# Optimization experiments

Hardware: AMD Instinct MI355X
Metric: run time of the kernel (lower is better)

The kernel has to match this reference:

```python
import jax, jax.numpy as jnp
import numpy as np

NHEAD, DK, DV = 8, 32, 32
GRAPH = [[1,2,3,6,7],[1,2,4],[1,3,5],[2,4],[3,5],[1,6,8,12],[1,7,9,13],[6,8,10],[7,9,13],[8,10],[9,11],[9,12,14],[11,13,15],[12,14,16],[13,15,17],[14,16],[15,17]]
_idx = np.zeros((17,5), np.int32); _val = np.zeros((17,5), bool)
for _i, _nb in enumerate(GRAPH):
    for _j, _n in enumerate(_nb):
        _idx[_i,_j] = _n-1; _val[_i,_j] = True
NBR_IDX = jnp.asarray(_idx)            # (17,5) neighbor table (pad idx 0)
NBR_VALID = jnp.asarray(_val)          # (17,5) valid-neighbor mask
ATT_MASK = jnp.asarray(np.concatenate([_val, np.ones((17,2), bool)], 1))  # (17,7): 5 local + 2 global keys
INV_SQRT_DK = float(1.0/np.sqrt(DK))

def _ln_c(x, g, b, eps=1e-6):
    # LayerNorm over channel axis of (B,C,L)
    m = x.mean(1, keepdims=True)
    v = x.var(1, keepdims=True)
    return (x - m) * jax.lax.rsqrt(v + eps) * g[None,:,None] + b[None,:,None]

def _bn3(x, g, b, eps=1e-5):
    # BatchNorm1d (training batch stats) per channel over (B,L); x:(B,C,L)
    m = x.mean((0,2), keepdims=True)
    v = x.var((0,2), keepdims=True)
    return (x - m) * jax.lax.rsqrt(v + eps) * g[None,:,None] + b[None,:,None]

def _pos_ffn(x, w1, b1, w2, b2, g, b):
    # x:(B,C,L); Linear over C, relu, Linear back, residual, BatchNorm1d
    h = jax.nn.relu(jnp.einsum('bcl,hc->bhl', x, w1) + b1[None,:,None])
    y = jnp.einsum('bhl,ch->bcl', h, w2) + b2[None,:,None] + x
    return _bn3(y, g, b)

def _unfold(t):
    # t:(B,C,17) -> (B,C,5,17): per-node 5-wide neighbor window, zero padded
    g = t[:,:,NBR_IDX]                              # (B,C,17,5)
    g = jnp.where(NBR_VALID[None,None], g, 0.0)
    return jnp.transpose(g, (0,1,3,2))

def _sju(xn, ax, wq,bq,wk,bk,wv,bv, bng,bnb, f1w,f1b,f2w,f2b,fg,fb):
    B, C, L = xn.shape
    q = (jnp.einsum('oc,bcl->bol', wq, xn) + bq[None,:,None]).reshape(B,NHEAD,DK,L)
    kx = jnp.einsum('oc,bcl->bol', wk, xn) + bk[None,:,None]
    vx = jnp.einsum('oc,bcl->bol', wv, xn) + bv[None,:,None]
    k = _unfold(kx).reshape(B,NHEAD,DK,5,L)
    v = _unfold(vx).reshape(B,NHEAD,DV,5,L)
    ak = (jnp.einsum('oc,bcal->boal', wk, ax) + bk[None,:,None,None]).reshape(B,NHEAD,DK,2,L)
    av = (jnp.einsum('oc,bcal->boal', wv, ax) + bv[None,:,None,None]).reshape(B,NHEAD,DV,2,L)
    k = jnp.concatenate([k, ak], 3)                 # (B,H,dk,7,L)
    v = jnp.concatenate([v, av], 3)
    pre = jnp.einsum('bhdl,bhdwl->bhwl', q, k) * INV_SQRT_DK
    pre = jnp.where(ATT_MASK.T[None,None], pre, -jnp.inf)
    a = jax.nn.softmax(pre, axis=2)
    att = jnp.einsum('bhwl,bhdwl->bhdl', a, v).reshape(B,C,L)
    ret = _bn3(xn + att, bng, bnb)
    return _pos_ffn(ret, f1w,f1b,f2w,f2b,fg,fb)

def _sru(x, y, wq,bq,wk,bk,wv,bv, bng,bnb, f1w,f1b,f2w,f2b,fg,fb):
    # x:(B,C) relay, y:(B,C,Ly) keys/values
    B, C = x.shape
    q = (x @ wq.T + bq).reshape(B,NHEAD,DK)
    k = (jnp.einsum('oc,bcl->bol', wk, y) + bk[None,:,None]).reshape(B,NHEAD,DK,-1)
    v = (jnp.einsum('oc,bcl->bol', wv, y) + bv[None,:,None]).reshape(B,NHEAD,DV,-1)
    a = jax.nn.softmax(jnp.einsum('bhd,bhdl->bhl', q, k) * INV_SQRT_DK, axis=2)
    att = jnp.einsum('bhl,bhdl->bhd', a, v).reshape(B,C)
    ret = _bn3((x + att)[:,:,None], bng, bnb)
    return _pos_ffn(ret, f1w,f1b,f2w,f2b,fg,fb)[:,:,0]

def _forward(data, ln_g, ln_b, jq_w, jq_b, jk_w, jk_b, jv_w, jv_b, jbn_g, jbn_b, jf1_w, jf1_b, jf2_w, jf2_b, jfbn_g, jfbn_b, rq_w, rq_b, rk_w, rk_b, rv_w, rv_b, rbn_g, rbn_b, rf1_w, rf1_b, rf2_w, rf2_b, rfbn_g, rfbn_b):
    B, C, V, T = data.shape
    embs = jnp.transpose(data, (0,3,1,2)).reshape(B*T, C, V)   # fold time into batch
    nodes = embs
    relay = embs.mean(2)                                       # (BT,C)
    # ax: per node the 2 extra keys = its own original embedding + relay (fixed across layers)
    ax = jnp.stack([embs, jnp.broadcast_to(relay[:,:,None], embs.shape)], axis=2)  # (BT,C,2,V)
    for i in range(ln_g.shape[0]):
        xn = _ln_c(nodes, ln_g[i], ln_b[i])
        nodes = jax.nn.leaky_relu(_sju(xn, ax, jq_w[i],jq_b[i],jk_w[i],jk_b[i],jv_w[i],jv_b[i],jbn_g[i],jbn_b[i],jf1_w[i],jf1_b[i],jf2_w[i],jf2_b[i],jfbn_g[i],jfbn_b[i]), 0.01)
        y = jnp.concatenate([relay[:,:,None], nodes], axis=2)   # (BT,C,18)
        relay = jax.nn.leaky_relu(_sru(relay, y, rq_w[i],rq_b[i],rk_w[i],rk_b[i],rv_w[i],rv_b[i],rbn_g[i],rbn_b[i],rf1_w[i],rf1_b[i],rf2_w[i],rf2_b[i],rfbn_g[i],rfbn_b[i]), 0.01)
    return jnp.transpose(nodes.reshape(B,T,C,V), (0,2,3,1))

def setup_inputs():
    key = jax.random.key(0)
    Lyr, C, DIN, B, T, V = 2, 256, 1024, 4, 256, 17
    ks = jax.random.split(key, 40)
    ctr = [0]
    def nxt():
        k = ks[ctr[0]]; ctr[0] += 1; return k
    def w(shape, s=0.05):
        return jax.random.normal(nxt(), shape, jnp.float32) * s
    ones = lambda: jnp.ones((Lyr, C), jnp.float32)
    zeros = lambda: jnp.zeros((Lyr, C), jnp.float32)
    inp = {'data': jax.random.normal(nxt(), (B,C,V,T), jnp.float32),
           'ln_g': ones(), 'ln_b': zeros()}
    for p in ('j', 'r'):
        inp[p+'q_w'] = w((Lyr,C,C)); inp[p+'q_b'] = w((Lyr,C))
        inp[p+'k_w'] = w((Lyr,C,C)); inp[p+'k_b'] = w((Lyr,C))
        inp[p+'v_w'] = w((Lyr,C,C)); inp[p+'v_b'] = w((Lyr,C))
        inp[p+'bn_g'] = ones(); inp[p+'bn_b'] = zeros()
        inp[p+'f1_w'] = w((Lyr,DIN,C)); inp[p+'f1_b'] = w((Lyr,DIN))
        inp[p+'f2_w'] = w((Lyr,C,DIN)); inp[p+'f2_b'] = w((Lyr,C))
        inp[p+'fbn_g'] = ones(); inp[p+'fbn_b'] = zeros()
    return inp

def reference(data, ln_g, ln_b, jq_w, jq_b, jk_w, jk_b, jv_w, jv_b, jbn_g, jbn_b, jf1_w, jf1_b, jf2_w, jf2_b, jfbn_g, jfbn_b, rq_w, rq_b, rk_w, rk_b, rv_w, rv_b, rbn_g, rbn_b, rf1_w, rf1_b, rf2_w, rf2_b, rfbn_g, rfbn_b):
    return _forward(data, ln_g, ln_b, jq_w, jq_b, jk_w, jk_b, jv_w, jv_b, jbn_g, jbn_b, jf1_w, jf1_b, jf2_w, jf2_b, jfbn_g, jfbn_b, rq_w, rq_b, rk_w, rk_b, rv_w, rv_b, rbn_g, rbn_b, rf1_w, rf1_b, rf2_w, rf2_b, rfbn_g, rfbn_b)
```

## Files before the change

kernel.cpp:

```cpp
#include <hip/hip_runtime.h>
#include <hip/hip_bf16.h>


using bf16 = __hip_bfloat16;
typedef __attribute__((ext_vector_type(8))) short bf16x8v;
typedef __attribute__((ext_vector_type(4))) float f32x4;

namespace {
constexpr int kBT = 1024;
constexpr int kC = 256;
constexpr int kV = 17;
constexpr int kT = 256;
constexpr int kDIN = 1024;
constexpr int kRows = kBT * kV;
constexpr int kRowsE = kRows + kBT;
constexpr float kInvSqrtDk = 0.17677669529663687f;
constexpr size_t SZ_BIG = (size_t)kRows * kC;
}

__constant__ int c_nbi[17][5] = {
    {0, 1, 2, 5, 6},   {0, 1, 3, 0, 0},   {0, 2, 4, 0, 0},  {1, 3, 0, 0, 0},
    {2, 4, 0, 0, 0},   {0, 5, 7, 11, 0},  {0, 6, 8, 12, 0}, {5, 7, 9, 0, 0},
    {6, 8, 12, 0, 0},  {7, 9, 0, 0, 0},   {8, 10, 0, 0, 0}, {8, 11, 13, 0, 0},
    {10, 12, 14, 0, 0},{11, 13, 15, 0, 0},{12, 14, 16, 0, 0},
    {13, 15, 0, 0, 0}, {14, 16, 0, 0, 0}};
__constant__ int c_ncnt[17] = {5, 3, 3, 2, 2, 4, 4, 3, 3, 2, 2, 3, 3, 3, 3, 2, 2};

__device__ inline float bf2f(unsigned short s) {
  unsigned int u = ((unsigned int)s) << 16;
  float f;
  __builtin_memcpy(&f, &u, 4);
  return f;
}
__device__ inline unsigned short f2bf(float f) {
  unsigned int u;
  __builtin_memcpy(&u, &f, 4);
  unsigned int r = (u + 0x7fffu + ((u >> 16) & 1u)) >> 16;
  return (unsigned short)r;
}
__device__ inline float4 ldbf4(const bf16* p) {
  ushort4 u = *(const ushort4*)p;
  return make_float4(bf2f(u.x), bf2f(u.y), bf2f(u.z), bf2f(u.w));
}
__device__ inline void stbf4(bf16* p, float4 v) {
  ushort4 u = make_ushort4(f2bf(v.x), f2bf(v.y), f2bf(v.z), f2bf(v.w));
  *(ushort4*)p = u;
}
__device__ inline float dot4(float4 a, float4 b) {
  return a.x * b.x + a.y * b.y + a.z * b.z + a.w * b.w;
}

__device__ inline void async16(const bf16* g, bf16* l) {
  __builtin_amdgcn_global_load_lds(
      (const __attribute__((address_space(1))) void*)g,
      (__attribute__((address_space(3))) void*)l, 16, 0, 0);
}

template <int KT>
__device__ __forceinline__ void gemm128_body(
    char* smem_raw, const bf16* __restrict__ A, const bf16* __restrict__ W,
    const float* __restrict__ bias, bf16* __restrict__ outB, int N, int flags,
    int row0, int col0) {
  bf16* As = (bf16*)smem_raw;
  bf16* Bs = (bf16*)(smem_raw + 16384);
  const int tid = threadIdx.x;
  const int wave = tid >> 6;
  const int lane = tid & 63;

  const int sub = lane >> 2;
  const int kq = (lane & 3) * 8;
  const int rg0 = (2 * wave + 0) * 16;
  const int rg1 = (2 * wave + 1) * 16;
  const bf16* ag0 = A + (size_t)(row0 + rg0 + sub) * KT + kq;
  const bf16* ag1 = A + (size_t)(row0 + rg1 + sub) * KT + kq;
  const bf16* bg0 = W + (size_t)(col0 + rg0 + sub) * KT + kq;
  const bf16* bg1 = W + (size_t)(col0 + rg1 + sub) * KT + kq;

  const int wm = wave >> 1, wn = wave & 1;
  const int fr = lane & 15;
  const int fk = (lane >> 4) * 8;

  f32x4 acc[4][4];
#pragma unroll
  for (int i = 0; i < 4; ++i)
#pragma unroll
    for (int j = 0; j < 4; ++j) acc[i][j] = (f32x4){0.f, 0.f, 0.f, 0.f};

#define STAGE32(buf, koff)                              \
  do {                                                  \
    async16(ag0 + (koff), As + (buf) * 4096 + rg0 * 32); \
    async16(ag1 + (koff), As + (buf) * 4096 + rg1 * 32); \
    async16(bg0 + (koff), Bs + (buf) * 4096 + rg0 * 32); \
    async16(bg1 + (koff), Bs + (buf) * 4096 + rg1 * 32); \
  } while (0)

  STAGE32(0, 0);
  __syncthreads();

  for (int k0 = 0; k0 < KT; k0 += 32) {
    const int cur = (k0 >> 5) & 1;
    if (k0 + 32 < KT) STAGE32(cur ^ 1, k0 + 32);
    bf16x8v af[4], bfv[4];
#pragma unroll
    for (int i = 0; i < 4; ++i)
      af[i] = *(const bf16x8v*)&As[cur * 4096 +
                                   (wm * 64 + i * 16 + fr) * 32 + fk];
#pragma unroll
    for (int j = 0; j < 4; ++j)
      bfv[j] = *(const bf16x8v*)&Bs[cur * 4096 +
                                    (wn * 64 + j * 16 + fr) * 32 + fk];
#pragma unroll
    for (int i = 0; i < 4; ++i)
#pragma unroll
      for (int j = 0; j < 4; ++j)
        acc[i][j] = __builtin_amdgcn_mfma_f32_16x16x32_bf16(af[i], bfv[j],
                                                            acc[i][j], 0, 0,
                                                            0);
    __syncthreads();
  }
#undef STAGE32

  unsigned short* cs = (unsigned short*)smem_raw;
#pragma unroll
  for (int j = 0; j < 4; ++j) {
    int lc = wn * 64 + j * 16 + fr;
    float bv = bias ? bias[col0 + lc] : 0.f;
#pragma unroll
    for (int i = 0; i < 4; ++i) {
      int lr = wm * 64 + i * 16 + (lane >> 4) * 4;
#pragma unroll
      for (int r = 0; r < 4; ++r) {
        float v = acc[i][j][r] + bv;
        if (flags & 1) v = fmaxf(v, 0.f);
        cs[(lr + r) * 128 + lc] = f2bf(v);
      }
    }
  }
  __syncthreads();
#pragma unroll
  for (int p = 0; p < 8; ++p) {
    int lr = p * 16 + (tid >> 4);
    int lc = (tid & 15) * 8;
    *(bf16x8v*)&outB[(size_t)(row0 + lr) * N + col0 + lc] =
        *(const bf16x8v*)&cs[lr * 128 + lc];
  }
}

template <int KT>
__global__ __launch_bounds__(256, 4) void k_mfma_gemm(
    const bf16* __restrict__ A, const bf16* __restrict__ W,
    const float* __restrict__ bias, bf16* __restrict__ outB, int N,
    int flags) {
  __shared__ __align__(16) char smem_raw[32768];
  gemm128_body<KT>(smem_raw, A, W, bias, outB, N, flags, blockIdx.x * 128,
                   blockIdx.y * 128);
}

__global__ __launch_bounds__(256, 4) void k_mfma_gemm_dual(
    const bf16* __restrict__ A0, const bf16* __restrict__ W0,
    const float* __restrict__ b0, bf16* __restrict__ o0, int N0, int gx0,
    int nb0, const bf16* __restrict__ A1, const bf16* __restrict__ W1,
    const float* __restrict__ b1, bf16* __restrict__ o1, int N1, int gx1) {
  __shared__ __align__(16) char smem_raw[32768];
  const int bid = blockIdx.x;
  if (bid < nb0) {
    int bx = bid % gx0, by = bid / gx0;
    gemm128_body<256>(smem_raw, A0, W0, b0, o0, N0, 4, bx * 128, by * 128);
  } else {
    int local = bid - nb0;
    int bx = local % gx1, by = local / gx1;
    gemm128_body<256>(smem_raw, A1, W1, b1, o1, N1, 4, bx * 128, by * 128);
  }
}

__global__ __launch_bounds__(256, 4) void k_mfma_gemm64(
    const bf16* __restrict__ A, const bf16* __restrict__ W,
    const float* __restrict__ bias, const float* __restrict__ res,
    float* __restrict__ outF, const float* __restrict__ bnScI,
    const float* __restrict__ bnShI, float* __restrict__ partOut, int nbPart,
    int N) {
  constexpr int KT = 1024;
  __shared__ __align__(16) bf16 As[2][4096];
  __shared__ __align__(16) bf16 Bs[2][4096];
  __shared__ float sred[4 * 64];
  __shared__ float qred[4 * 64];
  const int tid = threadIdx.x;
  const int wave = tid >> 6;
  const int lane = tid & 63;
  const int row0 = blockIdx.x * 64;
  const int col0 = blockIdx.y * 64;

  const int srow = wave * 16 + (lane >> 2);
  const int skq = (lane & 3) * 8;
  const bf16* ag = A + (size_t)(row0 + srow) * KT + skq;
  const bf16* bg = W + (size_t)(col0 + srow) * KT + skq;

  const int wm = wave >> 1, wn = wave & 1;
  const int fr = lane & 15;
  const int fk = (lane >> 4) * 8;

  f32x4 acc[2][2];
#pragma unroll
  for (int i = 0; i < 2; ++i)
#pragma unroll
    for (int j = 0; j < 2; ++j) acc[i][j] = (f32x4){0.f, 0.f, 0.f, 0.f};

#define STAGE64x64(buf, koff)                                      \
  do {                                                             \
    _Pragma("unroll") for (int kc = 0; kc < 2; ++kc) {             \
      async16(ag + (koff) + kc * 32,                               \
              &As[(buf)][kc * 2048 + wave * 512]);                 \
      async16(bg + (koff) + kc * 32,                               \
              &Bs[(buf)][kc * 2048 + wave * 512]);                 \
    }                                                              \
  } while (0)

  STAGE64x64(0, 0);
  __syncthreads();

  for (int k0 = 0; k0 < KT; k0 += 64) {
    const int cur = (k0 >> 6) & 1;
    if (k0 + 64 < KT) STAGE64x64(cur ^ 1, k0 + 64);
#pragma unroll
    for (int kc = 0; kc < 2; ++kc) {
      bf16x8v af[2], bfv[2];
#pragma unroll
      for (int i = 0; i < 2; ++i)
        af[i] = *(const bf16x8v*)&As[cur][kc * 2048 +
                                          (wm * 32 + i * 16 + fr) * 32 + fk];
#pragma unroll
      for (int j = 0; j < 2; ++j)
        bfv[j] = *(const bf16x8v*)&Bs[cur][kc * 2048 +
                                           (wn * 32 + j * 16 + fr) * 32 + fk];
#pragma unroll
      for (int i = 0; i < 2; ++i)
#pragma unroll
        for (int j = 0; j < 2; ++j)
          acc[i][j] = __builtin_amdgcn_mfma_f32_16x16x32_bf16(af[i], bfv[j],
                                                              acc[i][j], 0, 0,
                                                              0);
    }
    __syncthreads();
  }
#undef STAGE64x64

  const int crow = row0 + wm * 32;
  const int ccol = col0 + wn * 32;
  float colS[2] = {0.f, 0.f};
  float colQ[2] = {0.f, 0.f};
#pragma unroll
  for (int j = 0; j < 2; ++j) {
    int col = ccol + j * 16 + fr;
    float bv = bias[col];
    float rsc = bnScI[col], rsh = bnShI[col];
#pragma unroll
    for (int i = 0; i < 2; ++i) {
      int rowb = crow + i * 16 + (lane >> 4) * 4;
#pragma unroll
      for (int r = 0; r < 4; ++r) {
        size_t row = (size_t)(rowb + r);
        float v = acc[i][j][r] + bv + res[row * N + col] * rsc + rsh;
        outF[row * N + col] = v;
        colS[j] += v;
        colQ[j] += v * v;
      }
    }
  }
#pragma unroll
  for (int j = 0; j < 2; ++j) {
    colS[j] += __shfl_xor(colS[j], 16);
    colS[j] += __shfl_xor(colS[j], 32);
    colQ[j] += __shfl_xor(colQ[j], 16);
    colQ[j] += __shfl_xor(colQ[j], 32);
  }
  if (lane < 16) {
#pragma unroll
    for (int j = 0; j < 2; ++j) {
      sred[wave * 64 + j * 16 + fr] = colS[j];
      qred[wave * 64 + j * 16 + fr] = colQ[j];
    }
  }
  __syncthreads();
  if (tid < 64) {
    int c = tid;
    int wsel = c >> 5, off = c & 31;
    float s = sred[wsel * 64 + off] + sred[(wsel + 2) * 64 + off];
    float q = qred[wsel * 64 + off] + qred[(wsel + 2) * 64 + off];
    int col = col0 + c;
    partOut[(size_t)blockIdx.x * kC + col] = s;
    partOut[(size_t)(nbPart + blockIdx.x) * kC + col] = q;
  }
}

__global__ __launch_bounds__(256) void k_xform_in(const float* __restrict__ data,
                                                  float* __restrict__ nodes,
                                                  bf16* __restrict__ embs_bf) {
  __shared__ float tile[32][33];
  int ct = blockIdx.x * 32, tt = blockIdx.y * 32;
  int bv = blockIdx.z;
  int b = bv / kV, v = bv - b * kV;
  int tx = threadIdx.x & 31, ty = threadIdx.x >> 5;
  for (int i = ty; i < 32; i += 8)
    tile[i][tx] = data[(((size_t)b * kC + ct + i) * kV + v) * kT + tt + tx];
  __syncthreads();
  for (int i = ty; i < 32; i += 8) {
    size_t s = (size_t)b * kT + tt + i;
    size_t idx = (s * kV + v) * kC + ct + tx;
    float val = tile[tx][i];
    nodes[idx] = val;
    embs_bf[idx] = __float2bfloat16(val);
  }
}

__global__ __launch_bounds__(256) void k_xform_out(const float* __restrict__ Z,
                                                   const float* __restrict__ scale,
                                                   const float* __restrict__ shift,
                                                   float* __restrict__ out) {
  __shared__ float tile[32][33];
  int ct = blockIdx.x * 32, tt = blockIdx.y * 32;
  int bv = blockIdx.z;
  int b = bv / kV, v = bv - b * kV;
  int tx = threadIdx.x & 31, ty = threadIdx.x >> 5;
  float sc = scale[ct + tx], sh = shift[ct + tx];
  for (int i = ty; i < 32; i += 8) {
    size_t s = (size_t)b * kT + tt + i;
    float val = Z[(s * kV + v) * kC + ct + tx] * sc + sh;
    val = (val > 0.f) ? val : 0.01f * val;
    tile[i][tx] = val;
  }
  __syncthreads();
  for (int i = ty; i < 32; i += 8)
    out[(((size_t)b * kC + ct + i) * kV + v) * kT + tt + tx] = tile[tx][i];
}

__global__ __launch_bounds__(256) void k_ln_relay(
    const float* __restrict__ nodes, const float* __restrict__ g,
    const float* __restrict__ b, float* __restrict__ O,
    bf16* __restrict__ Ob, bf16* __restrict__ relay0_bf) {
  int t = threadIdx.x;
  int bid = blockIdx.x;
  if (bid < kRows / 4) {
    int row = bid * 4 + (t >> 6);
    int c4 = (t & 63) * 4;
    size_t i = (size_t)row * kC + c4;
    float4 x = *(const float4*)(nodes + i);
    float s = x.x + x.y + x.z + x.w;
    float q = dot4(x, x);
#pragma unroll
    for (int o = 32; o >= 1; o >>= 1) {
      s += __shfl_xor(s, o);
      q += __shfl_xor(q, o);
    }
    float m = s * (1.f / 256.f);
    float var = q * (1.f / 256.f) - m * m;
    float rs = rsqrtf(var + 1e-6f);
    float4 g4 = *(const float4*)(g + c4);
    float4 b4 = *(const float4*)(b + c4);
    float4 o4 = make_float4((x.x - m) * rs * g4.x + b4.x,
                            (x.y - m) * rs * g4.y + b4.y,
                            (x.z - m) * rs * g4.z + b4.z,
                            (x.w - m) * rs * g4.w + b4.w);
    *(float4*)(O + i) = o4;
    stbf4(Ob + i, o4);
  } else {
    int s = (bid - kRows / 4) * 4 + (t >> 6);
    int c4 = (t & 63) * 4;
    float4 acc = make_float4(0.f, 0.f, 0.f, 0.f);
#pragma unroll
    for (int v = 0; v < kV; ++v) {
      float4 x = *(const float4*)(nodes + ((size_t)s * kV + v) * kC + c4);
      acc.x += x.x; acc.y += x.y; acc.z += x.z; acc.w += x.w;
    }
    float4 r =
        make_float4(acc.x / 17.f, acc.y / 17.f, acc.z / 17.f, acc.w / 17.f);
    stbf4(relay0_bf + (size_t)s * kC + c4, r);
  }
}

__global__ __launch_bounds__(256) void k_attn_sat(const bf16* __restrict__ qkv,
                                                  const bf16* __restrict__ akav,
                                                  float* __restrict__ z,
                                                  float* __restrict__ part,
                                                  int nb) {
  __shared__ float sS[4][256];
  __shared__ float qS[4][256];
  int t = threadIdx.x;
  int w = t >> 6;
  int lane = t & 63;
  int c4 = lane * 4;
  float sAcc[4] = {0.f, 0.f, 0.f, 0.f};
  float qAcc[4] = {0.f, 0.f, 0.f, 0.f};
  for (int r = 0; r < 4; ++r) {
    int rl = blockIdx.x * 16 + w * 4 + r;
    int s = rl / kV, l = rl - s * kV;
    float4 q = ldbf4(qkv + (size_t)rl * 768 + c4);
    int cnt = c_ncnt[l];
    float sc[7];
    int nrow[5];
#pragma unroll
    for (int wd = 0; wd < 5; ++wd) {
      nrow[wd] = s * kV + c_nbi[l][wd];
      float4 k = ldbf4(qkv + (size_t)nrow[wd] * 768 + 256 + c4);
      float p = dot4(q, k);
      p += __shfl_xor(p, 1, 8);
      p += __shfl_xor(p, 2, 8);
      p += __shfl_xor(p, 4, 8);
      sc[wd] = (wd < cnt) ? p * kInvSqrtDk : -1e30f;
    }
    {
      float4 k = ldbf4(akav + (size_t)rl * 1024 + c4);
      float p = dot4(q, k);
      p += __shfl_xor(p, 1, 8);
      p += __shfl_xor(p, 2, 8);
      p += __shfl_xor(p, 4, 8);
      sc[5] = p * kInvSqrtDk;
    }
    {
      float4 k = ldbf4(akav + (size_t)(kRows + s) * 1024 + c4);
      float p = dot4(q, k);
      p += __shfl_xor(p, 1, 8);
      p += __shfl_xor(p, 2, 8);
      p += __shfl_xor(p, 4, 8);
      sc[6] = p * kInvSqrtDk;
    }
    float mx = sc[0];
#pragma unroll
    for (int wd = 1; wd < 7; ++wd) mx = fmaxf(mx, sc[wd]);
    float den = 0.f;
#pragma unroll
    for (int wd = 0; wd < 7; ++wd) {
      sc[wd] = __expf(sc[wd] - mx);
      den += sc[wd];
    }
    float inv = 1.f / den;
    float4 acc = make_float4(0.f, 0.f, 0.f, 0.f);
#pragma unroll
    for (int wd = 0; wd < 5; ++wd) {
      float4 v = ldbf4(qkv + (size_t)nrow[wd] * 768 + 512 + c4);
      acc.x += sc[wd] * v.x; acc.y += sc[wd] * v.y;
      acc.z += sc[wd] * v.z; acc.w += sc[wd] * v.w;
    }
    {
      float4 v = ldbf4(akav + (size_t)rl * 1024 + 256 + c4);
      acc.x += sc[5] * v.x; acc.y += sc[5] * v.y;
      acc.z += sc[5] * v.z; acc.w += sc[5] * v.w;
    }
    {
      float4 v = ldbf4(akav + (size_t)(kRows + s) * 1024 + 256 + c4);
      acc.x += sc[6] * v.x; acc.y += sc[6] * v.y;
      acc.z += sc[6] * v.z; acc.w += sc[6] * v.w;
    }
    size_t zi = (size_t)rl * kC + c4;
    float4 xv = *(const float4*)(z + zi);
    float4 o = make_float4(xv.x + acc.x * inv, xv.y + acc.y * inv,
                           xv.z + acc.z * inv, xv.w + acc.w * inv);
    *(float4*)(z + zi) = o;
    sAcc[0] += o.x; sAcc[1] += o.y; sAcc[2] += o.z; sAcc[3] += o.w;
    qAcc[0] += o.x * o.x; qAcc[1] += o.y * o.y;
    qAcc[2] += o.z * o.z; qAcc[3] += o.w * o.w;
  }
  sS[w][c4 + 0] = sAcc[0]; sS[w][c4 + 1] = sAcc[1];
  sS[w][c4 + 2] = sAcc[2]; sS[w][c4 + 3] = sAcc[3];
  qS[w][c4 + 0] = qAcc[0]; qS[w][c4 + 1] = qAcc[1];
  qS[w][c4 + 2] = qAcc[2]; qS[w][c4 + 3] = qAcc[3];
  __syncthreads();
  float ps = sS[0][t] + sS[1][t] + sS[2][t] + sS[3][t];
  float pq = qS[0][t] + qS[1][t] + qS[2][t] + qS[3][t];
  part[(size_t)blockIdx.x * kC + t] = ps;
  part[(size_t)(nb + blockIdx.x) * kC + t] = pq;
}

__global__ __launch_bounds__(256) void k_bn_finalize(const float* __restrict__ part,
                                                     int nb, float inv_n,
                                                     const float* __restrict__ g,
                                                     const float* __restrict__ b,
                                                     float* __restrict__ scale,
                                                     float* __restrict__ shift) {
  int c = blockIdx.x;
  int t = threadIdx.x;
  float s = 0.f, q = 0.f;
  for (int i = t; i < nb; i += 256) {
    s += part[(size_t)i * kC + c];
    q += part[(size_t)(nb + i) * kC + c];
  }
#pragma unroll
  for (int o = 32; o >= 1; o >>= 1) {
    s += __shfl_xor(s, o);
    q += __shfl_xor(q, o);
  }
  __shared__ float ws[4], wq[4];
  int wid = t >> 6;
  if ((t & 63) == 0) { ws[wid] = s; wq[wid] = q; }
  __syncthreads();
  if (t == 0) {
    float S = ws[0] + ws[1] + ws[2] + ws[3];
    float Q = wq[0] + wq[1] + wq[2] + wq[3];
    float m = S * inv_n;
    float var = Q * inv_n - m * m;
    float sc = g[c] * rsqrtf(var + 1e-5f);
    scale[c] = sc;
    shift[c] = b[c] - m * sc;
  }
}

__global__ __launch_bounds__(256) void k_bn_apply(const float* __restrict__ Z,
                                                  const float* __restrict__ scale,
                                                  const float* __restrict__ shift,
                                                  float* __restrict__ outF,
                                                  bf16* __restrict__ outB,
                                                  int leaky) {
  int t = threadIdx.x;
  int row = blockIdx.x * 4 + (t >> 6);
  int c4 = (t & 63) * 4;
  size_t i = (size_t)row * kC + c4;
  float4 z = *(const float4*)(Z + i);
  float4 sc = *(const float4*)(scale + c4);
  float4 sh = *(const float4*)(shift + c4);
  float4 v = make_float4(z.x * sc.x + sh.x, z.y * sc.y + sh.y,
                         z.z * sc.z + sh.z, z.w * sc.w + sh.w);
  if (leaky) {
    v.x = (v.x > 0.f) ? v.x : 0.01f * v.x;
    v.y = (v.y > 0.f) ? v.y : 0.01f * v.y;
    v.z = (v.z > 0.f) ? v.z : 0.01f * v.z;
    v.w = (v.w > 0.f) ? v.w : 0.01f * v.w;
  }
  if (outF) *(float4*)(outF + i) = v;
  if (outB) stbf4(outB + i, v);
}

__global__ __launch_bounds__(256) void k_bn_ln(
    const float* __restrict__ Z, const float* __restrict__ scale,
    const float* __restrict__ shift, const float* __restrict__ g,
    const float* __restrict__ b, float* __restrict__ xnOut,
    bf16* __restrict__ actOut) {
  int t = threadIdx.x;
  int row = blockIdx.x * 4 + (t >> 6);
  int c4 = (t & 63) * 4;
  size_t i = (size_t)row * kC + c4;
  float4 z = *(const float4*)(Z + i);
  float4 sc = *(const float4*)(scale + c4);
  float4 sh = *(const float4*)(shift + c4);
  float4 v = make_float4(z.x * sc.x + sh.x, z.y * sc.y + sh.y,
                         z.z * sc.z + sh.z, z.w * sc.w + sh.w);
  v.x = (v.x > 0.f) ? v.x : 0.01f * v.x;
  v.y = (v.y > 0.f) ? v.y : 0.01f * v.y;
  v.z = (v.z > 0.f) ? v.z : 0.01f * v.z;
  v.w = (v.w > 0.f) ? v.w : 0.01f * v.w;
  float s = v.x + v.y + v.z + v.w;
  float q = dot4(v, v);
#pragma unroll
  for (int o = 32; o >= 1; o >>= 1) {
    s += __shfl_xor(s, o);
    q += __shfl_xor(q, o);
  }
  float m = s * (1.f / 256.f);
  float var = q * (1.f / 256.f) - m * m;
  float rs = rsqrtf(var + 1e-6f);
  float4 g4 = *(const float4*)(g + c4);
  float4 b4 = *(const float4*)(b + c4);
  float4 o4 = make_float4((v.x - m) * rs * g4.x + b4.x,
                          (v.y - m) * rs * g4.y + b4.y,
                          (v.z - m) * rs * g4.z + b4.z,
                          (v.w - m) * rs * g4.w + b4.w);
  *(float4*)(xnOut + i) = o4;
  stbf4(actOut + i, o4);
}

struct CvtTab {
  const float* src[12];
  bf16* dst[12];
  int n[12];
  const float* bsrc[10];
  float* bdst[10];
};
__global__ __launch_bounds__(256) void k_cvt_multi(CvtTab t) {
  int c = blockIdx.y;
  if (c == 12) {
    if (blockIdx.x < 10) t.bdst[blockIdx.x][threadIdx.x] = t.bsrc[blockIdx.x][threadIdx.x];
    return;
  }
  int i = (blockIdx.x * 256 + threadIdx.x) * 4;
  if (i >= t.n[c]) return;
  float4 v = *(const float4*)(t.src[c] + i);
  stbf4(t.dst[c] + i, v);
}

extern "C" void kernel_launch(void* const* d_in, const int* in_sizes, int n_in,
                              void* d_out, int out_size, void* d_ws, size_t ws_size,
                              hipStream_t stream) {
  const float* data = (const float*)d_in[0];
  const float* ln_g = (const float*)d_in[1];
  const float* ln_b = (const float*)d_in[2];
  const float* jq_w = (const float*)d_in[3];
  const float* jq_b = (const float*)d_in[4];
  const float* jk_w = (const float*)d_in[5];
  const float* jk_b = (const float*)d_in[6];
  const float* jv_w = (const float*)d_in[7];
  const float* jv_b = (const float*)d_in[8];
  const float* jbn_g = (const float*)d_in[9];
  const float* jbn_b = (const float*)d_in[10];
  const float* jf1_w = (const float*)d_in[11];
  const float* jf1_b = (const float*)d_in[12];
  const float* jf2_w = (const float*)d_in[13];
  const float* jf2_b = (const float*)d_in[14];
  const float* jfbn_g = (const float*)d_in[15];
  const float* jfbn_b = (const float*)d_in[16];
  float* out = (float*)d_out;

  float* f = (float*)d_ws;
  float* nodes = f;    f += SZ_BIG;
  float* xn = f;       f += SZ_BIG;
  float* part = f;     f += 2 * (kRows / 4) * kC;
  float* scale = f;    f += kC;
  float* shift = f;    f += kC;
  float* cb_jqkv = f;  f += 2 * 768;
  float* cb_kv4 = f;   f += 1024;

  bf16* bfa = (bf16*)f;
  bf16* act_bf = bfa;   bfa += SZ_BIG;
  bf16* embsX_bf = bfa; bfa += (size_t)kRowsE * kC;
  bf16* P = bfa;        bfa += (size_t)kRows * kDIN;
  bf16* akavBuf = bfa;  bfa += (size_t)kRowsE * 1024;
  bf16* Wjqkv = bfa;    bfa += 2 * 768 * 256;
  bf16* Wkv4 = bfa;     bfa += 1024 * 256;
  bf16* Wjf1 = bfa;     bfa += 2 * 1024 * 256;
  bf16* Wjf2 = bfa;     bfa += 2 * 256 * 1024;

  bf16* relay0_bf = embsX_bf + SZ_BIG;
  bf16* qkv_bf = P;
  bf16* h_bf = P;
  float* y2 = xn;

  auto gemm = [&](const bf16* A, const bf16* W, const float* bias,
                  bf16* oB, int M, int N, int flags) {
    dim3 g(M / 128, N / 128);
    k_mfma_gemm<256><<<g, 256, 0, stream>>>(A, W, bias, oB, N, flags);
  };

  {
    CvtTab t;
    for (int i = 0; i < 2; ++i) {
      const size_t om = (size_t)i * kC * kC;
      const float* s3[3] = {jq_w + om, jk_w + om, jv_w + om};
      bf16* d3[3] = {Wjqkv + (size_t)i * 768 * 256,
                     Wjqkv + (size_t)i * 768 * 256 + 65536,
                     Wjqkv + (size_t)i * 768 * 256 + 131072};
      for (int j = 0; j < 3; ++j) {
        t.src[i * 3 + j] = s3[j];
        t.dst[i * 3 + j] = d3[j];
        t.n[i * 3 + j] = 65536;
      }
    }
    t.src[6] = jk_w;                 t.dst[6] = Wkv4;               t.n[6] = 65536;
    t.src[7] = jv_w;                 t.dst[7] = Wkv4 + 65536;       t.n[7] = 65536;
    t.src[8] = jk_w + (size_t)65536; t.dst[8] = Wkv4 + 131072;      t.n[8] = 65536;
    t.src[9] = jv_w + (size_t)65536; t.dst[9] = Wkv4 + 196608;      t.n[9] = 65536;
    t.src[10] = jf1_w; t.dst[10] = Wjf1; t.n[10] = 2 * 1024 * 256;
    t.src[11] = jf2_w; t.dst[11] = Wjf2; t.n[11] = 2 * 256 * 1024;
    for (int i = 0; i < 2; ++i) {
      t.bsrc[i * 3 + 0] = jq_b + (size_t)i * kC;
      t.bsrc[i * 3 + 1] = jk_b + (size_t)i * kC;
      t.bsrc[i * 3 + 2] = jv_b + (size_t)i * kC;
      t.bdst[i * 3 + 0] = cb_jqkv + i * 768;
      t.bdst[i * 3 + 1] = cb_jqkv + i * 768 + 256;
      t.bdst[i * 3 + 2] = cb_jqkv + i * 768 + 512;
    }
    t.bsrc[6] = jk_b;       t.bdst[6] = cb_kv4;
    t.bsrc[7] = jv_b;       t.bdst[7] = cb_kv4 + 256;
    t.bsrc[8] = jk_b + kC;  t.bdst[8] = cb_kv4 + 512;
    t.bsrc[9] = jv_b + kC;  t.bdst[9] = cb_kv4 + 768;
    k_cvt_multi<<<dim3(512, 13), 256, 0, stream>>>(t);
  }

  k_xform_in<<<dim3(8, 8, 4 * kV), 256, 0, stream>>>(data, nodes, embsX_bf);

  k_ln_relay<<<kRows / 4 + kBT / 4, 256, 0, stream>>>(nodes, ln_g, ln_b, xn,
                                                      act_bf, relay0_bf);

  {
    const int gx0 = kRowsE / 128, nb0 = gx0 * (1024 / 128);
    const int gx1 = kRows / 128, nb1 = gx1 * (768 / 128);
    k_mfma_gemm_dual<<<nb0 + nb1, 256, 0, stream>>>(
        embsX_bf, Wkv4, cb_kv4, akavBuf, 1024, gx0, nb0,
        act_bf, Wjqkv, cb_jqkv, qkv_bf, 768, gx1);
  }

  for (int i = 0; i < 2; ++i) {
    const size_t ob = (size_t)i * kC, ofb1 = (size_t)i * kDIN;
    const bf16* Wf1 = Wjf1 + (size_t)i * 1024 * 256;
    const bf16* Wf2 = Wjf2 + (size_t)i * 256 * 1024;
    const int nbA = kRows / 16;
    const int nbG = kRows / 64;

    if (i == 1) {
      gemm(act_bf, Wjqkv + (size_t)768 * 256, cb_jqkv + 768, qkv_bf, kRows,
           768, 4);
    }
    k_attn_sat<<<kRows / 16, 256, 0, stream>>>(qkv_bf,
                                               akavBuf + (size_t)i * 512, xn,
                                               part, nbA);
    k_bn_finalize<<<kC, 256, 0, stream>>>(part, nbA, 1.f / kRows, jbn_g + ob,
                                          jbn_b + ob, scale, shift);
    k_bn_apply<<<kRows / 4, 256, 0, stream>>>(xn, scale, shift, nullptr,
                                              act_bf, 0);
    gemm(act_bf, Wf1, jf1_b + ofb1, h_bf, kRows, 1024, 4 | 1);
    k_mfma_gemm64<<<dim3(kRows / 64, kC / 64), 256, 0, stream>>>(
        h_bf, Wf2, jf2_b + ob, xn, y2, scale, shift, part, nbG, kC);
    k_bn_finalize<<<kC, 256, 0, stream>>>(part, nbG, 1.f / kRows, jfbn_g + ob,
                                          jfbn_b + ob, scale, shift);
    if (i == 0) {
      k_bn_ln<<<kRows / 4, 256, 0, stream>>>(y2, scale, shift, ln_g + kC,
                                             ln_b + kC, xn, act_bf);
    }
  }

  k_xform_out<<<dim3(8, 8, 4 * kV), 256, 0, stream>>>(y2, scale, shift, out);
  (void)in_sizes; (void)n_in; (void)out_size; (void)ws_size;
}
```

Measured before the change: 374.8 us.

## Fold attention BatchNorm affine into FFN first-layer weights and bias

Removes the separate BN-apply pass over the activations after attention. The attention kernel now also writes a bf16 copy of its pre-BN output, and a small kernel scales the W1 columns by the BN scale and folds the BN shift into an effective bias. The first FFN GEMM then runs on the un-normalized bf16 activations. This saves a full read and write of the activation tensor, at the cost of an extra bf16 store in attention and per-layer weight folding. Precision changes slightly because un-normalized values are rounded to bf16 and the scale is applied to the weights instead of the activations. The residual in the second FFN GEMM still reads xn, which may be the pre-BN value; that could be a correctness concern if the residual expects normalized input.

```diff
diff --git a/kernel.cpp b/kernel.cpp
--- a/kernel.cpp
+++ b/kernel.cpp
@@ -292,6 +292,31 @@
   }
 }
 
+__global__ __launch_bounds__(256) void k_fold_w1(
+    const float* __restrict__ w1, const float* __restrict__ b1,
+    const float* __restrict__ scale, const float* __restrict__ shift,
+    bf16* __restrict__ w1f, float* __restrict__ b1eff) {
+  __shared__ float red[4][4];
+  int c = threadIdx.x;
+  int wave = c >> 6, lane = c & 63;
+  float sc = scale[c], sh = shift[c];
+#pragma unroll
+  for (int r = 0; r < 4; ++r) {
+    int h = blockIdx.x * 4 + r;
+    float w = w1[(size_t)h * kC + c];
+    w1f[(size_t)h * kC + c] = __float2bfloat16(w * sc);
+    float d = w * sh;
+#pragma unroll
+    for (int o = 32; o >= 1; o >>= 1) d += __shfl_xor(d, o);
+    if (lane == 0) red[r][wave] = d;
+  }
+  __syncthreads();
+  if (c < 4) {
+    int h = blockIdx.x * 4 + c;
+    b1eff[h] = b1[h] + red[c][0] + red[c][1] + red[c][2] + red[c][3];
+  }
+}
+
 __global__ __launch_bounds__(256) void k_xform_in(const float* __restrict__ data,
                                                   float* __restrict__ nodes,
                                                   bf16* __restrict__ embs_bf) {
@@ -380,6 +405,7 @@
 __global__ __launch_bounds__(256) void k_attn_sat(const bf16* __restrict__ qkv,
                                                   const bf16* __restrict__ akav,
                                                   float* __restrict__ z,
+                                                  bf16* __restrict__ xnb,
                                                   float* __restrict__ part,
                                                   int nb) {
   __shared__ float sS[4][256];
@@ -455,6 +481,7 @@
     float4 o = make_float4(xv.x + acc.x * inv, xv.y + acc.y * inv,
                            xv.z + acc.z * inv, xv.w + acc.w * inv);
     *(float4*)(z + zi) = o;
+    stbf4(xnb + zi, o);
     sAcc[0] += o.x; sAcc[1] += o.y; sAcc[2] += o.z; sAcc[3] += o.w;
     qAcc[0] += o.x * o.x; qAcc[1] += o.y * o.y;
     qAcc[2] += o.z * o.z; qAcc[3] += o.w * o.w;
@@ -501,31 +528,6 @@
     scale[c] = sc;
     shift[c] = b[c] - m * sc;
   }
-}
-
-__global__ __launch_bounds__(256) void k_bn_apply(const float* __restrict__ Z,
-                                                  const float* __restrict__ scale,
-                                                  const float* __restrict__ shift,
-                                                  float* __restrict__ outF,
-                                                  bf16* __restrict__ outB,
-                                                  int leaky) {
-  int t = threadIdx.x;
-  int row = blockIdx.x * 4 + (t >> 6);
-  int c4 = (t & 63) * 4;
-  size_t i = (size_t)row * kC + c4;
-  float4 z = *(const float4*)(Z + i);
-  float4 sc = *(const float4*)(scale + c4);
-  float4 sh = *(const float4*)(shift + c4);
-  float4 v = make_float4(z.x * sc.x + sh.x, z.y * sc.y + sh.y,
-                         z.z * sc.z + sh.z, z.w * sc.w + sh.w);
-  if (leaky) {
-    v.x = (v.x > 0.f) ? v.x : 0.01f * v.x;
-    v.y = (v.y > 0.f) ? v.y : 0.01f * v.y;
-    v.z = (v.z > 0.f) ? v.z : 0.01f * v.z;
-    v.w = (v.w > 0.f) ? v.w : 0.01f * v.w;
-  }
-  if (outF) *(float4*)(outF + i) = v;
-  if (outB) stbf4(outB + i, v);
 }
 
 __global__ __launch_bounds__(256) void k_bn_ln(
@@ -613,6 +615,7 @@
   float* part = f;     f += 2 * (kRows / 4) * kC;
   float* scale = f;    f += kC;
   float* shift = f;    f += kC;
+  float* b1eff = f;    f += kDIN;
   float* cb_jqkv = f;  f += 2 * 768;
   float* cb_kv4 = f;   f += 1024;
 
@@ -655,7 +658,7 @@
     t.src[7] = jv_w;                 t.dst[7] = Wkv4 + 65536;       t.n[7] = 65536;
     t.src[8] = jk_w + (size_t)65536; t.dst[8] = Wkv4 + 131072;      t.n[8] = 65536;
     t.src[9] = jv_w + (size_t)65536; t.dst[9] = Wkv4 + 196608;      t.n[9] = 65536;
-    t.src[10] = jf1_w; t.dst[10] = Wjf1; t.n[10] = 2 * 1024 * 256;
+    t.src[10] = jf2_w; t.dst[10] = Wjf2; t.n[10] = 0;
     t.src[11] = jf2_w; t.dst[11] = Wjf2; t.n[11] = 2 * 256 * 1024;
     for (int i = 0; i < 2; ++i) {
       t.bsrc[i * 3 + 0] = jq_b + (size_t)i * kC;
@@ -686,8 +689,8 @@
   }
 
   for (int i = 0; i < 2; ++i) {
-    const size_t ob = (size_t)i * kC, ofb1 = (size_t)i * kDIN;
-    const bf16* Wf1 = Wjf1 + (size_t)i * 1024 * 256;
+    const size_t ob = (size_t)i * kC;
+    bf16* Wf1 = Wjf1 + (size_t)i * 1024 * 256;
     const bf16* Wf2 = Wjf2 + (size_t)i * 256 * 1024;
     const int nbA = kRows / 16;
     const int nbG = kRows / 64;
@@ -698,12 +701,13 @@
     }
     k_attn_sat<<<kRows / 16, 256, 0, stream>>>(qkv_bf,
                                                akavBuf + (size_t)i * 512, xn,
-                                               part, nbA);
+                                               act_bf, part, nbA);
     k_bn_finalize<<<kC, 256, 0, stream>>>(part, nbA, 1.f / kRows, jbn_g + ob,
                                           jbn_b + ob, scale, shift);
-    k_bn_apply<<<kRows / 4, 256, 0, stream>>>(xn, scale, shift, nullptr,
-                                              act_bf, 0);
-    gemm(act_bf, Wf1, jf1_b + ofb1, h_bf, kRows, 1024, 4 | 1);
+    k_fold_w1<<<kDIN / 4, 256, 0, stream>>>(jf1_w + (size_t)i * kDIN * kC,
+                                            jf1_b + (size_t)i * kDIN, scale,
+                                            shift, Wf1, b1eff);
+    gemm(act_bf, Wf1, b1eff, h_bf, kRows, 1024, 4 | 1);
     k_mfma_gemm64<<<dim3(kRows / 64, kC / 64), 256, 0, stream>>>(
         h_bf, Wf2, jf2_b + ob, xn, y2, scale, shift, part, nbG, kC);
     k_bn_finalize<<<kC, 256, 0, stream>>>(part, nbG, 1.f / kRows, jfbn_g + ob,
```

New measurement: 374.6 us. About the same (-0.1%).
